# Optimization experiments

Measured on AMD Instinct MI355X. Metric: run time of the kernel, lower is better.

Reference implementation:

```python
import jax, jax.numpy as jnp
import numpy as np


def setup_inputs() -> dict:
    key = jax.random.key(0)
    ks = jax.random.split(key, 9)
    B, Cr, H, W = 16, 1024, 28, 28
    Cs, Hs, Ws = 256, 25, 25  # Hs == Ws so adaptive pool == mean over width
    Ci = 512
    return {
        "x_rgb": jax.random.normal(ks[0], (B, Cr, H, W), jnp.float32),
        "x_skel": jax.random.normal(ks[1], (B, Cs, Hs, Ws), jnp.float32),
        "Wq": jax.random.normal(ks[2], (Ci, Cr), jnp.float32) * (Cr ** -0.5),
        "bq": jax.random.normal(ks[3], (Ci,), jnp.float32) * 0.01,
        "Wk": jax.random.normal(ks[4], (Ci, Cs), jnp.float32) * (Cs ** -0.5),
        "bk": jax.random.normal(ks[5], (Ci,), jnp.float32) * 0.01,
        "Wv": jax.random.normal(ks[6], (Cr, Cs), jnp.float32) * (Cs ** -0.5),
        "bv": jax.random.normal(ks[7], (Cr,), jnp.float32) * 0.01,
        "gamma": jax.random.normal(ks[8], (1,), jnp.float32) * 0.1,
    }


def reference(x_rgb, x_skel, Wq, bq, Wk, bk, Wv, bv, gamma):
    B, Cr, H, W = x_rgb.shape
    Ws = x_skel.shape[3]
    # adaptive_avg_pool2d(x_skel, (Ws, 1)) with Hs == Ws -> mean over width
    pooled = jnp.mean(x_skel, axis=3)  # [B, Cs, Ws]
    # 1x1 conv projections as matmuls
    q = jnp.einsum('ic,bchw->bihw', Wq, x_rgb) + bq[None, :, None, None]
    q = q.reshape(B, -1, H * W).transpose(0, 2, 1)          # [B, HW, Ci]
    k = jnp.einsum('ic,bcs->bis', Wk, pooled) + bk[None, :, None]  # [B, Ci, Ws]
    energy = jnp.einsum('bni,bis->bns', q, k)               # [B, HW, Ws]
    attention = jax.nn.softmax(energy, axis=-1)             # [B, HW, Ws]
    v = jnp.einsum('rc,bcs->brs', Wv, pooled) + bv[None, :, None]  # [B, Cr, Ws]
    out = jnp.einsum('brs,bns->brn', v, attention)          # [B, Cr, HW]
    out = out.reshape(B, Cr, H, W)
    return gamma[0] * out + x_rgb
```

## Files before the change

kernel.cpp:

```cpp
#include <hip/hip_runtime.h>

#define BB 16
#define CR 1024
#define HWD 784
#define HW2 392
#define CS 256
#define SSZ 25
#define SP 28
#define CI 512
#define CSPLIT 8
#define CCHUNK 128
#define RSPLIT 32
#define RCHUNK 32
#define KC 4

#define OFF_POOLED 0
#define OFF_VP     102400
#define OFF_MP     561152
#define OFF_E0     1019904
#define OFF_ATT    1020304
#define OFF_EP     1333904
#define OFF_KK     1333904
#define OFF_P      1563280

__global__ __launch_bounds__(256) void k_pool(const float* __restrict__ xs,
                                              float* __restrict__ pooled) {
    __shared__ float buf[4][400];
    int wave = threadIdx.x >> 6, lane = threadIdx.x & 63;
    int r0 = blockIdx.x * 64 + wave * 16;
    const float4* src = (const float4*)(xs + (size_t)r0 * SSZ);
    float4* b4 = (float4*)buf[wave];
    b4[lane] = src[lane];
    if (lane < 36) b4[64 + lane] = src[64 + lane];
    __syncthreads();
    if (lane < 16) {
        const float* row = buf[wave] + lane * SSZ;
        float s = 0.f;
#pragma unroll
        for (int w = 0; w < SSZ; ++w) s += row[w];
        pooled[r0 + lane] = s * (1.0f / SSZ);
    }
}

template <int NS>
__device__ __forceinline__ void proj_body(const float* __restrict__ wrow,
                                          const float* __restrict__ pb, int s0,
                                          float bias, float* __restrict__ dst,
                                          bool zpad) {
    float acc[NS];
#pragma unroll
    for (int i = 0; i < NS; ++i) acc[i] = 0.f;
    const float4* w4 = (const float4*)wrow;
#pragma unroll 4
    for (int c4 = 0; c4 < CS / 4; ++c4) {
        float4 w = w4[c4];
        const float* p = pb + c4 * 4 * SSZ + s0;
#pragma unroll
        for (int i = 0; i < NS; ++i)
            acc[i] = fmaf(w.x, p[i],
                     fmaf(w.y, p[SSZ + i],
                     fmaf(w.z, p[2 * SSZ + i],
                     fmaf(w.w, p[3 * SSZ + i], acc[i]))));
    }
#pragma unroll
    for (int i = 0; i < NS; ++i) dst[s0 + i] = acc[i] + bias;
    if (zpad) { dst[25] = 0.f; dst[26] = 0.f; dst[27] = 0.f; }
}

__global__ __launch_bounds__(256) void k_kkv(const float* __restrict__ Wk,
                                             const float* __restrict__ Wv,
                                             const float* __restrict__ bk,
                                             const float* __restrict__ bv,
                                             const float* __restrict__ pooled,
                                             float* __restrict__ kk,
                                             float* __restrict__ vp) {
    int rb = blockIdx.x >> 2, sh = blockIdx.x & 3;
    int b = blockIdx.y;
    const float* pb = pooled + (size_t)b * CS * SSZ;
    const float* wrow;
    float bias;
    float* dst;
    if (rb < 2) {
        int i = rb * 256 + threadIdx.x;
        wrow = Wk + (size_t)i * CS;
        bias = bk[i];
        dst = kk + ((size_t)b * CI + i) * SP;
    } else {
        int r = (rb - 2) * 256 + threadIdx.x;
        wrow = Wv + (size_t)r * CS;
        bias = bv[r];
        dst = vp + ((size_t)b * CR + r) * SP;
    }
    int s0 = sh * 7;
    if (sh < 3) proj_body<7>(wrow, pb, s0, bias, dst, false);
    else        proj_body<4>(wrow, pb, s0, bias, dst, true);
}

__global__ __launch_bounds__(256) void k_Mpart(const float* __restrict__ Wq,
                                               const float* __restrict__ kk,
                                               float* __restrict__ P) {
    __shared__ __align__(16) float lds[128 * 8];
    int sh = blockIdx.x, kc = blockIdx.y, b = blockIdx.z;
    int t = threadIdx.x;
    int s0 = sh * 7;
    int i0 = kc * 128;
    const float* kkb = kk + (size_t)b * CI * SP;
#pragma unroll
    for (int q = 0; q < 4; ++q) {
        int d = t + 256 * q;
        lds[d] = kkb[(size_t)(i0 + (d >> 3)) * SP + s0 + (d & 7)];
    }
    __syncthreads();

    float acc[28];
#pragma unroll
    for (int e = 0; e < 28; ++e) acc[e] = 0.f;
    const float4* lds4 = (const float4*)lds;
#pragma unroll 4
    for (int i = 0; i < 128; ++i) {
        float4 w = *(const float4*)(Wq + (size_t)(i0 + i) * CR + 4 * t);
        float4 k0 = lds4[i * 2];
        float4 k1 = lds4[i * 2 + 1];
#pragma unroll
        for (int j = 0; j < 4; ++j) {
            float wj = j == 0 ? w.x : j == 1 ? w.y : j == 2 ? w.z : w.w;
            acc[j * 7 + 0] = fmaf(wj, k0.x, acc[j * 7 + 0]);
            acc[j * 7 + 1] = fmaf(wj, k0.y, acc[j * 7 + 1]);
            acc[j * 7 + 2] = fmaf(wj, k0.z, acc[j * 7 + 2]);
            acc[j * 7 + 3] = fmaf(wj, k0.w, acc[j * 7 + 3]);
            acc[j * 7 + 4] = fmaf(wj, k1.x, acc[j * 7 + 4]);
            acc[j * 7 + 5] = fmaf(wj, k1.y, acc[j * 7 + 5]);
            acc[j * 7 + 6] = fmaf(wj, k1.z, acc[j * 7 + 6]);
        }
    }
    float* dst = P + ((((size_t)kc * BB + b) * 4 + sh) * 256 + t) * 28;
#pragma unroll
    for (int m = 0; m < 7; ++m) {
        float4 o;
        o.x = acc[4 * m + 0]; o.y = acc[4 * m + 1];
        o.z = acc[4 * m + 2]; o.w = acc[4 * m + 3];
        *(float4*)(dst + 4 * m) = o;
    }
}

__global__ __launch_bounds__(256) void k_Mred(const float* __restrict__ P,
                                              float* __restrict__ Mp) {
    int id = blockIdx.x * 256 + threadIdx.x;
    int t = id & 255, sh = (id >> 8) & 3, b = id >> 10;
    const float* p0 = P + ((((size_t)b) * 4 + sh) * 256 + t) * 28;
    const size_t PL = (size_t)BB * 4 * 256 * 28;
    float v[28];
#pragma unroll
    for (int m = 0; m < 7; ++m) {
        float4 a = *(const float4*)(p0 + 4 * m);
        float4 b1 = *(const float4*)(p0 + PL + 4 * m);
        float4 c = *(const float4*)(p0 + 2 * PL + 4 * m);
        float4 d = *(const float4*)(p0 + 3 * PL + 4 * m);
        v[4 * m + 0] = a.x + b1.x + c.x + d.x;
        v[4 * m + 1] = a.y + b1.y + c.y + d.y;
        v[4 * m + 2] = a.z + b1.z + c.z + d.z;
        v[4 * m + 3] = a.w + b1.w + c.w + d.w;
    }
    int s0 = sh * 7;
    float* mb = Mp + ((size_t)b * CR + 4 * t) * SP + s0;
#pragma unroll
    for (int j = 0; j < 4; ++j)
#pragma unroll
        for (int u = 0; u < 7; ++u)
            mb[j * SP + u] = v[j * 7 + u];
}

__global__ __launch_bounds__(64) void k_e0(const float* __restrict__ bq,
                                           const float* __restrict__ kk,
                                           float* __restrict__ e0) {
    int s = blockIdx.x, b = blockIdx.y;
    int l = threadIdx.x;
    const float* kb = kk + (size_t)b * CI * SP;
    float a = 0.f;
#pragma unroll
    for (int k = 0; k < CI / 64; ++k) {
        int i = l + 64 * k;
        a = fmaf(bq[i], kb[(size_t)i * SP + s], a);
    }
#pragma unroll
    for (int off = 32; off > 0; off >>= 1) a += __shfl_down(a, off);
    if (l == 0) e0[b * SSZ + s] = a;
}

__global__ __launch_bounds__(64) void k_energy(const float* __restrict__ xr,
                                               const float* __restrict__ Mp,
                                               float* __restrict__ Ep) {
    __shared__ float ldsM[CCHUNK * SP];
    int lane = threadIdx.x;
    int b = blockIdx.y, ch = blockIdx.z;
    int cbeg = ch * CCHUNK;
    {
        const float4* src = (const float4*)(Mp + ((size_t)b * CR + cbeg) * SP);
        float4* dst = (float4*)ldsM;
#pragma unroll
        for (int j = 0; j < 14; ++j) dst[lane + 64 * j] = src[lane + 64 * j];
    }
    __syncthreads();

    int n2 = blockIdx.x * 64 + lane;
    bool valid = n2 < HW2;
    int n2c = valid ? n2 : 0;
    const float2* x2 = (const float2*)(xr + (size_t)b * CR * HWD);

    float acc0[SP], acc1[SP];
#pragma unroll
    for (int s = 0; s < SP; ++s) { acc0[s] = 0.f; acc1[s] = 0.f; }

    for (int c = 0; c < CCHUNK; c += 4) {
        float2 xv[4];
#pragma unroll
        for (int u = 0; u < 4; ++u)
            xv[u] = x2[(size_t)(cbeg + c + u) * HW2 + n2c];
#pragma unroll
        for (int u = 0; u < 4; ++u) {
            const float4* mr = (const float4*)&ldsM[(c + u) * SP];
#pragma unroll
            for (int j = 0; j < 7; ++j) {
                float4 m = mr[j];
                acc0[4 * j + 0] = fmaf(xv[u].x, m.x, acc0[4 * j + 0]);
                acc0[4 * j + 1] = fmaf(xv[u].x, m.y, acc0[4 * j + 1]);
                acc0[4 * j + 2] = fmaf(xv[u].x, m.z, acc0[4 * j + 2]);
                acc0[4 * j + 3] = fmaf(xv[u].x, m.w, acc0[4 * j + 3]);
                acc1[4 * j + 0] = fmaf(xv[u].y, m.x, acc1[4 * j + 0]);
                acc1[4 * j + 1] = fmaf(xv[u].y, m.y, acc1[4 * j + 1]);
                acc1[4 * j + 2] = fmaf(xv[u].y, m.z, acc1[4 * j + 2]);
                acc1[4 * j + 3] = fmaf(xv[u].y, m.w, acc1[4 * j + 3]);
            }
        }
    }
    if (valid) {
        float2* ep = (float2*)Ep + ((size_t)(ch * BB + b) * SSZ) * HW2 + n2;
#pragma unroll
        for (int s = 0; s < SSZ; ++s) ep[(size_t)s * HW2] = make_float2(acc0[s], acc1[s]);
    }
}

__global__ __launch_bounds__(64) void k_softmax(const float* __restrict__ Ep,
                                                const float* __restrict__ e0,
                                                float* __restrict__ att) {
    int lane = threadIdx.x;
    int n2 = blockIdx.x * 64 + lane;
    int b = blockIdx.y;
    if (n2 >= HW2) return;
    float ex[SSZ], ey[SSZ];
#pragma unroll
    for (int s = 0; s < SSZ; ++s) { float v = e0[b * SSZ + s]; ex[s] = v; ey[s] = v; }
    const float2* ep2 = (const float2*)Ep;
    for (int ch = 0; ch < CSPLIT; ++ch) {
        const float2* ep = ep2 + ((size_t)(ch * BB + b) * SSZ) * HW2 + n2;
#pragma unroll
        for (int s = 0; s < SSZ; ++s) {
            float2 v = ep[(size_t)s * HW2];
            ex[s] += v.x; ey[s] += v.y;
        }
    }
    float mx = ex[0], my = ey[0];
#pragma unroll
    for (int s = 1; s < SSZ; ++s) { mx = fmaxf(mx, ex[s]); my = fmaxf(my, ey[s]); }
    float sx = 0.f, sy = 0.f;
#pragma unroll
    for (int s = 0; s < SSZ; ++s) {
        ex[s] = __expf(ex[s] - mx); sx += ex[s];
        ey[s] = __expf(ey[s] - my); sy += ey[s];
    }
    float ix = 1.0f / sx, iy = 1.0f / sy;
    float2* ao = (float2*)att + ((size_t)b * SSZ) * HW2 + n2;
#pragma unroll
    for (int s = 0; s < SSZ; ++s) ao[(size_t)s * HW2] = make_float2(ex[s] * ix, ey[s] * iy);
}

__global__ __launch_bounds__(64) void k_out(const float* __restrict__ xr,
                                            const float* __restrict__ vp,
                                            const float* __restrict__ att,
                                            const float* __restrict__ gamma,
                                            float* __restrict__ out) {
    __shared__ float ldsv[RCHUNK * SP];
    int lane = threadIdx.x;
    int b = blockIdx.y, rz = blockIdx.z;
    int r0 = rz * RCHUNK;
    {
        const float4* src = (const float4*)(vp + ((size_t)b * CR + r0) * SP);
        float4* dst = (float4*)ldsv;
#pragma unroll
        for (int j = 0; j < 4; ++j) {
            int idx = lane + 64 * j;
            if (idx < RCHUNK * SP / 4) dst[idx] = src[idx];
        }
    }
    __syncthreads();

    int n2 = blockIdx.x * 64 + lane;
    bool valid = n2 < HW2;
    int n2c = valid ? n2 : 0;

    float a0[SP], a1[SP];
    const float2* at2 = (const float2*)att + ((size_t)b * SSZ) * HW2 + n2c;
#pragma unroll
    for (int s = 0; s < SSZ; ++s) {
        float2 av = at2[(size_t)s * HW2];
        a0[s] = av.x; a1[s] = av.y;
    }
#pragma unroll
    for (int s = SSZ; s < SP; ++s) { a0[s] = 0.f; a1[s] = 0.f; }

    float g = gamma[0];
    const float2* x2 = (const float2*)(xr + (size_t)b * CR * HWD);
    float2* o2 = (float2*)(out + (size_t)b * CR * HWD);

#pragma unroll 4
    for (int r = 0; r < RCHUNK; ++r) {
        float2 xv = x2[(size_t)(r0 + r) * HW2 + n2c];
        float d0 = 0.f, d1 = 0.f;
        const float4* vr = (const float4*)&ldsv[r * SP];
#pragma unroll
        for (int j = 0; j < 7; ++j) {
            float4 v = vr[j];
            d0 = fmaf(v.x, a0[4 * j + 0], d0);
            d0 = fmaf(v.y, a0[4 * j + 1], d0);
            d0 = fmaf(v.z, a0[4 * j + 2], d0);
            d0 = fmaf(v.w, a0[4 * j + 3], d0);
            d1 = fmaf(v.x, a1[4 * j + 0], d1);
            d1 = fmaf(v.y, a1[4 * j + 1], d1);
            d1 = fmaf(v.z, a1[4 * j + 2], d1);
            d1 = fmaf(v.w, a1[4 * j + 3], d1);
        }
        if (valid)
            o2[(size_t)(r0 + r) * HW2 + n2] = make_float2(fmaf(g, d0, xv.x), fmaf(g, d1, xv.y));
    }
}

extern "C" void kernel_launch(void* const* d_in, const int* in_sizes, int n_in,
                              void* d_out, int out_size, void* d_ws, size_t ws_size,
                              hipStream_t stream) {
    const float* x_rgb  = (const float*)d_in[0];
    const float* x_skel = (const float*)d_in[1];
    const float* Wq     = (const float*)d_in[2];
    const float* bq     = (const float*)d_in[3];
    const float* Wk     = (const float*)d_in[4];
    const float* bk     = (const float*)d_in[5];
    const float* Wv     = (const float*)d_in[6];
    const float* bv     = (const float*)d_in[7];
    const float* gamma  = (const float*)d_in[8];
    float* out = (float*)d_out;

    float* ws     = (float*)d_ws;
    float* pooled = ws + OFF_POOLED;
    float* vp     = ws + OFF_VP;
    float* Mp     = ws + OFF_MP;
    float* e0     = ws + OFF_E0;
    float* att    = ws + OFF_ATT;
    float* Ep     = ws + OFF_EP;
    float* kk     = ws + OFF_KK;
    float* P      = ws + OFF_P;

    k_pool   <<<dim3(1600),           256, 0, stream>>>(x_skel, pooled);
    k_kkv    <<<dim3(24, 16),         256, 0, stream>>>(Wk, Wv, bk, bv, pooled, kk, vp);
    k_Mpart  <<<dim3(4, KC, 16),      256, 0, stream>>>(Wq, kk, P);
    k_Mred   <<<dim3(64),             256, 0, stream>>>(P, Mp);
    k_e0     <<<dim3(25, 16),          64, 0, stream>>>(bq, kk, e0);
    k_energy <<<dim3(7, 16, CSPLIT),   64, 0, stream>>>(x_rgb, Mp, Ep);
    k_softmax<<<dim3(7, 16),           64, 0, stream>>>(Ep, e0, att);
    k_out    <<<dim3(7, 16, RSPLIT),   64, 0, stream>>>(x_rgb, vp, att, gamma, out);
}
```

Measured before the change: 241.3 us.

## Fuse all stages into one persistent kernel with software grid barriers

Replaces eight separate kernel launches with a single 1024-block kernel that runs each stage in turn and separates them with an atomic-counter grid barrier. The aim is to remove per-launch overhead and the idle gaps between small dependent kernels. Blocks change from 64 to 256 threads for the energy and output stages, and the pooling stage now reads rows directly without staging them in LDS. In exchange, every block must spin at each barrier, the barrier is only correct if all 1024 blocks are resident at once, and its bounded spin can exit early and break ordering.

```diff
diff --git a/kernel.cpp b/kernel.cpp
--- a/kernel.cpp
+++ b/kernel.cpp
@@ -10,9 +10,9 @@
 #define CI 512
 #define CSPLIT 8
 #define CCHUNK 128
-#define RSPLIT 32
 #define RCHUNK 32
 #define KC 4
+#define NBLK 1024
 
 #define OFF_POOLED 0
 #define OFF_VP     102400
@@ -22,24 +22,26 @@
 #define OFF_EP     1333904
 #define OFF_KK     1333904
 #define OFF_P      1563280
-
-__global__ __launch_bounds__(256) void k_pool(const float* __restrict__ xs,
-                                              float* __restrict__ pooled) {
-    __shared__ float buf[4][400];
-    int wave = threadIdx.x >> 6, lane = threadIdx.x & 63;
-    int r0 = blockIdx.x * 64 + wave * 16;
-    const float4* src = (const float4*)(xs + (size_t)r0 * SSZ);
-    float4* b4 = (float4*)buf[wave];
-    b4[lane] = src[lane];
-    if (lane < 36) b4[64 + lane] = src[64 + lane];
+#define OFF_BAR    3842704
+
+__device__ __forceinline__ void gbar(unsigned* bar) {
     __syncthreads();
-    if (lane < 16) {
-        const float* row = buf[wave] + lane * SSZ;
-        float s = 0.f;
-#pragma unroll
-        for (int w = 0; w < SSZ; ++w) s += row[w];
-        pooled[r0 + lane] = s * (1.0f / SSZ);
-    }
+    if (threadIdx.x == 0) {
+        unsigned g = __hip_atomic_load(bar + 1, __ATOMIC_RELAXED, __HIP_MEMORY_SCOPE_AGENT);
+        unsigned a = __hip_atomic_fetch_add(bar, 1u, __ATOMIC_ACQ_REL, __HIP_MEMORY_SCOPE_AGENT);
+        if (a == (unsigned)(NBLK - 1)) {
+            __hip_atomic_store(bar, 0u, __ATOMIC_RELAXED, __HIP_MEMORY_SCOPE_AGENT);
+            __hip_atomic_fetch_add(bar + 1, 1u, __ATOMIC_RELEASE, __HIP_MEMORY_SCOPE_AGENT);
+        } else {
+            int spins = 0;
+            while (__hip_atomic_load(bar + 1, __ATOMIC_RELAXED, __HIP_MEMORY_SCOPE_AGENT) == g) {
+                __builtin_amdgcn_s_sleep(1);
+                if (++spins > (1 << 22)) break;
+            }
+        }
+        __threadfence();
+    }
+    __syncthreads();
 }
 
 template <int NS>
@@ -67,270 +69,281 @@
     if (zpad) { dst[25] = 0.f; dst[26] = 0.f; dst[27] = 0.f; }
 }
 
-__global__ __launch_bounds__(256) void k_kkv(const float* __restrict__ Wk,
-                                             const float* __restrict__ Wv,
-                                             const float* __restrict__ bk,
-                                             const float* __restrict__ bv,
-                                             const float* __restrict__ pooled,
-                                             float* __restrict__ kk,
-                                             float* __restrict__ vp) {
-    int rb = blockIdx.x >> 2, sh = blockIdx.x & 3;
-    int b = blockIdx.y;
-    const float* pb = pooled + (size_t)b * CS * SSZ;
-    const float* wrow;
-    float bias;
-    float* dst;
-    if (rb < 2) {
-        int i = rb * 256 + threadIdx.x;
-        wrow = Wk + (size_t)i * CS;
-        bias = bk[i];
-        dst = kk + ((size_t)b * CI + i) * SP;
-    } else {
-        int r = (rb - 2) * 256 + threadIdx.x;
-        wrow = Wv + (size_t)r * CS;
-        bias = bv[r];
-        dst = vp + ((size_t)b * CR + r) * SP;
-    }
-    int s0 = sh * 7;
-    if (sh < 3) proj_body<7>(wrow, pb, s0, bias, dst, false);
-    else        proj_body<4>(wrow, pb, s0, bias, dst, true);
-}
-
-__global__ __launch_bounds__(256) void k_Mpart(const float* __restrict__ Wq,
-                                               const float* __restrict__ kk,
-                                               float* __restrict__ P) {
-    __shared__ __align__(16) float lds[128 * 8];
-    int sh = blockIdx.x, kc = blockIdx.y, b = blockIdx.z;
-    int t = threadIdx.x;
-    int s0 = sh * 7;
-    int i0 = kc * 128;
-    const float* kkb = kk + (size_t)b * CI * SP;
-#pragma unroll
-    for (int q = 0; q < 4; ++q) {
-        int d = t + 256 * q;
-        lds[d] = kkb[(size_t)(i0 + (d >> 3)) * SP + s0 + (d & 7)];
-    }
-    __syncthreads();
-
-    float acc[28];
-#pragma unroll
-    for (int e = 0; e < 28; ++e) acc[e] = 0.f;
-    const float4* lds4 = (const float4*)lds;
+__global__ __launch_bounds__(256, 4) void mega(
+    const float* __restrict__ xr, const float* __restrict__ xs,
+    const float* __restrict__ Wq, const float* __restrict__ bq,
+    const float* __restrict__ Wk, const float* __restrict__ bk,
+    const float* __restrict__ Wv, const float* __restrict__ bv,
+    const float* __restrict__ gm, float* __restrict__ out,
+    float* __restrict__ ws)
+{
+    __shared__ __align__(16) float lds[CCHUNK * SP];
+
+    float* pooled = ws + OFF_POOLED;
+    float* vp     = ws + OFF_VP;
+    float* Mp     = ws + OFF_MP;
+    float* e0     = ws + OFF_E0;
+    float* att    = ws + OFF_ATT;
+    float* Ep     = ws + OFF_EP;
+    float* kk     = ws + OFF_KK;
+    float* P      = ws + OFF_P;
+    unsigned* bar = (unsigned*)(ws + OFF_BAR);
+
+    const int tid  = threadIdx.x;
+    const int wave = tid >> 6, lane = tid & 63;
+    const int bid  = blockIdx.x;
+
+    {
+        int id = bid * 256 + tid;
+        if (id < BB * CS * SSZ) {
+            const float* row = xs + (size_t)id * SSZ;
+            float s = 0.f;
+#pragma unroll
+            for (int w = 0; w < SSZ; ++w) s += row[w];
+            pooled[id] = s * (1.0f / SSZ);
+        }
+    }
+    gbar(bar);
+
+    if (bid < 24 * BB) {
+        int xx = bid % 24, b = bid / 24;
+        int rb = xx >> 2, sh = xx & 3;
+        const float* pb = pooled + (size_t)b * CS * SSZ;
+        const float* wrow; float bias; float* dst;
+        if (rb < 2) {
+            int i = rb * 256 + tid;
+            wrow = Wk + (size_t)i * CS; bias = bk[i];
+            dst  = kk + ((size_t)b * CI + i) * SP;
+        } else {
+            int r = (rb - 2) * 256 + tid;
+            wrow = Wv + (size_t)r * CS; bias = bv[r];
+            dst  = vp + ((size_t)b * CR + r) * SP;
+        }
+        int s0 = sh * 7;
+        if (sh < 3) proj_body<7>(wrow, pb, s0, bias, dst, false);
+        else        proj_body<4>(wrow, pb, s0, bias, dst, true);
+    }
+    gbar(bar);
+
+    if (bid < 4 * KC * BB) {
+        int sh = bid & 3, kc = (bid >> 2) & 3, b = bid >> 4;
+        int s0 = sh * 7, i0 = kc * 128;
+        const float* kkb = kk + (size_t)b * CI * SP;
+#pragma unroll
+        for (int q = 0; q < 4; ++q) {
+            int d = tid + 256 * q;
+            lds[d] = kkb[(size_t)(i0 + (d >> 3)) * SP + s0 + (d & 7)];
+        }
+        __syncthreads();
+        float acc[28];
+#pragma unroll
+        for (int e = 0; e < 28; ++e) acc[e] = 0.f;
+        const float4* lds4 = (const float4*)lds;
 #pragma unroll 4
-    for (int i = 0; i < 128; ++i) {
-        float4 w = *(const float4*)(Wq + (size_t)(i0 + i) * CR + 4 * t);
-        float4 k0 = lds4[i * 2];
-        float4 k1 = lds4[i * 2 + 1];
-#pragma unroll
-        for (int j = 0; j < 4; ++j) {
-            float wj = j == 0 ? w.x : j == 1 ? w.y : j == 2 ? w.z : w.w;
-            acc[j * 7 + 0] = fmaf(wj, k0.x, acc[j * 7 + 0]);
-            acc[j * 7 + 1] = fmaf(wj, k0.y, acc[j * 7 + 1]);
-            acc[j * 7 + 2] = fmaf(wj, k0.z, acc[j * 7 + 2]);
-            acc[j * 7 + 3] = fmaf(wj, k0.w, acc[j * 7 + 3]);
-            acc[j * 7 + 4] = fmaf(wj, k1.x, acc[j * 7 + 4]);
-            acc[j * 7 + 5] = fmaf(wj, k1.y, acc[j * 7 + 5]);
-            acc[j * 7 + 6] = fmaf(wj, k1.z, acc[j * 7 + 6]);
-        }
-    }
-    float* dst = P + ((((size_t)kc * BB + b) * 4 + sh) * 256 + t) * 28;
-#pragma unroll
-    for (int m = 0; m < 7; ++m) {
-        float4 o;
-        o.x = acc[4 * m + 0]; o.y = acc[4 * m + 1];
-        o.z = acc[4 * m + 2]; o.w = acc[4 * m + 3];
-        *(float4*)(dst + 4 * m) = o;
-    }
-}
-
-__global__ __launch_bounds__(256) void k_Mred(const float* __restrict__ P,
-                                              float* __restrict__ Mp) {
-    int id = blockIdx.x * 256 + threadIdx.x;
-    int t = id & 255, sh = (id >> 8) & 3, b = id >> 10;
-    const float* p0 = P + ((((size_t)b) * 4 + sh) * 256 + t) * 28;
-    const size_t PL = (size_t)BB * 4 * 256 * 28;
-    float v[28];
-#pragma unroll
-    for (int m = 0; m < 7; ++m) {
-        float4 a = *(const float4*)(p0 + 4 * m);
-        float4 b1 = *(const float4*)(p0 + PL + 4 * m);
-        float4 c = *(const float4*)(p0 + 2 * PL + 4 * m);
-        float4 d = *(const float4*)(p0 + 3 * PL + 4 * m);
-        v[4 * m + 0] = a.x + b1.x + c.x + d.x;
-        v[4 * m + 1] = a.y + b1.y + c.y + d.y;
-        v[4 * m + 2] = a.z + b1.z + c.z + d.z;
-        v[4 * m + 3] = a.w + b1.w + c.w + d.w;
-    }
-    int s0 = sh * 7;
-    float* mb = Mp + ((size_t)b * CR + 4 * t) * SP + s0;
-#pragma unroll
-    for (int j = 0; j < 4; ++j)
-#pragma unroll
-        for (int u = 0; u < 7; ++u)
-            mb[j * SP + u] = v[j * 7 + u];
-}
-
-__global__ __launch_bounds__(64) void k_e0(const float* __restrict__ bq,
-                                           const float* __restrict__ kk,
-                                           float* __restrict__ e0) {
-    int s = blockIdx.x, b = blockIdx.y;
-    int l = threadIdx.x;
-    const float* kb = kk + (size_t)b * CI * SP;
-    float a = 0.f;
-#pragma unroll
-    for (int k = 0; k < CI / 64; ++k) {
-        int i = l + 64 * k;
-        a = fmaf(bq[i], kb[(size_t)i * SP + s], a);
-    }
-#pragma unroll
-    for (int off = 32; off > 0; off >>= 1) a += __shfl_down(a, off);
-    if (l == 0) e0[b * SSZ + s] = a;
-}
-
-__global__ __launch_bounds__(64) void k_energy(const float* __restrict__ xr,
-                                               const float* __restrict__ Mp,
-                                               float* __restrict__ Ep) {
-    __shared__ float ldsM[CCHUNK * SP];
-    int lane = threadIdx.x;
-    int b = blockIdx.y, ch = blockIdx.z;
-    int cbeg = ch * CCHUNK;
+        for (int i = 0; i < 128; ++i) {
+            float4 w = *(const float4*)(Wq + (size_t)(i0 + i) * CR + 4 * tid);
+            float4 k0 = lds4[i * 2];
+            float4 k1 = lds4[i * 2 + 1];
+#pragma unroll
+            for (int j = 0; j < 4; ++j) {
+                float wj = j == 0 ? w.x : j == 1 ? w.y : j == 2 ? w.z : w.w;
+                acc[j * 7 + 0] = fmaf(wj, k0.x, acc[j * 7 + 0]);
+                acc[j * 7 + 1] = fmaf(wj, k0.y, acc[j * 7 + 1]);
+                acc[j * 7 + 2] = fmaf(wj, k0.z, acc[j * 7 + 2]);
+                acc[j * 7 + 3] = fmaf(wj, k0.w, acc[j * 7 + 3]);
+                acc[j * 7 + 4] = fmaf(wj, k1.x, acc[j * 7 + 4]);
+                acc[j * 7 + 5] = fmaf(wj, k1.y, acc[j * 7 + 5]);
+                acc[j * 7 + 6] = fmaf(wj, k1.z, acc[j * 7 + 6]);
+            }
+        }
+        float* dstP = P + ((((size_t)kc * BB + b) * 4 + sh) * 256 + tid) * 28;
+#pragma unroll
+        for (int m = 0; m < 7; ++m) {
+            float4 o;
+            o.x = acc[4 * m + 0]; o.y = acc[4 * m + 1];
+            o.z = acc[4 * m + 2]; o.w = acc[4 * m + 3];
+            *(float4*)(dstP + 4 * m) = o;
+        }
+    }
+    gbar(bar);
+
+    if (bid < 64) {
+        int id = bid * 256 + tid;
+        int t = id & 255, sh = (id >> 8) & 3, b = id >> 10;
+        const float* p0 = P + ((((size_t)b) * 4 + sh) * 256 + t) * 28;
+        const size_t PL = (size_t)BB * 4 * 256 * 28;
+        float vv[28];
+#pragma unroll
+        for (int m = 0; m < 7; ++m) {
+            float4 a  = *(const float4*)(p0 + 4 * m);
+            float4 b1 = *(const float4*)(p0 + PL + 4 * m);
+            float4 c  = *(const float4*)(p0 + 2 * PL + 4 * m);
+            float4 d  = *(const float4*)(p0 + 3 * PL + 4 * m);
+            vv[4 * m + 0] = a.x + b1.x + c.x + d.x;
+            vv[4 * m + 1] = a.y + b1.y + c.y + d.y;
+            vv[4 * m + 2] = a.z + b1.z + c.z + d.z;
+            vv[4 * m + 3] = a.w + b1.w + c.w + d.w;
+        }
+        int s0 = sh * 7;
+        float* mb = Mp + ((size_t)b * CR + 4 * t) * SP + s0;
+#pragma unroll
+        for (int j = 0; j < 4; ++j)
+#pragma unroll
+            for (int u = 0; u < 7; ++u)
+                mb[j * SP + u] = vv[j * 7 + u];
+    } else if (bid < 164) {
+        int wtask = (bid - 64) * 4 + wave;
+        int s = wtask % 25, b = wtask / 25;
+        const float* kb = kk + (size_t)b * CI * SP;
+        float a = 0.f;
+#pragma unroll
+        for (int k = 0; k < CI / 64; ++k) {
+            int i = lane + 64 * k;
+            a = fmaf(bq[i], kb[(size_t)i * SP + s], a);
+        }
+#pragma unroll
+        for (int off = 32; off > 0; off >>= 1) a += __shfl_down(a, off);
+        if (lane == 0) e0[b * SSZ + s] = a;
+    }
+    gbar(bar);
+
+    if (bid < 2 * CSPLIT * BB) {
+        int nq = bid & 1, ch = (bid >> 1) & 7, b = bid >> 4;
+        int cbeg = ch * CCHUNK;
+        {
+            const float4* src = (const float4*)(Mp + ((size_t)b * CR + cbeg) * SP);
+            float4* dst = (float4*)lds;
+#pragma unroll
+            for (int j = 0; j < 4; ++j) {
+                int idx = tid + 256 * j;
+                if (idx < CCHUNK * SP / 4) dst[idx] = src[idx];
+            }
+        }
+        __syncthreads();
+        int u = nq * 4 + wave;
+        if (u < 7) {
+            int n2 = u * 64 + lane;
+            bool valid = n2 < HW2;
+            int n2c = valid ? n2 : 0;
+            const float2* x2 = (const float2*)(xr + (size_t)b * CR * HWD);
+            float acc0[SP], acc1[SP];
+#pragma unroll
+            for (int s = 0; s < SP; ++s) { acc0[s] = 0.f; acc1[s] = 0.f; }
+            for (int c = 0; c < CCHUNK; c += 8) {
+                float2 xv[8];
+#pragma unroll
+                for (int q = 0; q < 8; ++q)
+                    xv[q] = x2[(size_t)(cbeg + c + q) * HW2 + n2c];
+#pragma unroll
+                for (int q = 0; q < 8; ++q) {
+                    const float4* mr = (const float4*)&lds[(c + q) * SP];
+#pragma unroll
+                    for (int j = 0; j < 7; ++j) {
+                        float4 m = mr[j];
+                        acc0[4 * j + 0] = fmaf(xv[q].x, m.x, acc0[4 * j + 0]);
+                        acc0[4 * j + 1] = fmaf(xv[q].x, m.y, acc0[4 * j + 1]);
+                        acc0[4 * j + 2] = fmaf(xv[q].x, m.z, acc0[4 * j + 2]);
+                        acc0[4 * j + 3] = fmaf(xv[q].x, m.w, acc0[4 * j + 3]);
+                        acc1[4 * j + 0] = fmaf(xv[q].y, m.x, acc1[4 * j + 0]);
+                        acc1[4 * j + 1] = fmaf(xv[q].y, m.y, acc1[4 * j + 1]);
+                        acc1[4 * j + 2] = fmaf(xv[q].y, m.z, acc1[4 * j + 2]);
+                        acc1[4 * j + 3] = fmaf(xv[q].y, m.w, acc1[4 * j + 3]);
+                    }
+                }
+            }
+            if (valid) {
+                float2* ep = (float2*)Ep + ((size_t)(ch * BB + b) * SSZ) * HW2 + n2;
+#pragma unroll
+                for (int s = 0; s < SSZ; ++s)
+                    ep[(size_t)s * HW2] = make_float2(acc0[s], acc1[s]);
+            }
+        }
+    }
+    gbar(bar);
+
+    if (bid < 28) {
+        int wtask = bid * 4 + wave;
+        int nb = wtask % 7, b = wtask / 7;
+        int n2 = nb * 64 + lane;
+        if (n2 < HW2) {
+            float ex[SSZ], ey[SSZ];
+#pragma unroll
+            for (int s = 0; s < SSZ; ++s) { float v = e0[b * SSZ + s]; ex[s] = v; ey[s] = v; }
+            const float2* ep2 = (const float2*)Ep;
+            for (int ch = 0; ch < CSPLIT; ++ch) {
+                const float2* ep = ep2 + ((size_t)(ch * BB + b) * SSZ) * HW2 + n2;
+#pragma unroll
+                for (int s = 0; s < SSZ; ++s) {
+                    float2 v = ep[(size_t)s * HW2];
+                    ex[s] += v.x; ey[s] += v.y;
+                }
+            }
+            float mx = ex[0], my = ey[0];
+#pragma unroll
+            for (int s = 1; s < SSZ; ++s) { mx = fmaxf(mx, ex[s]); my = fmaxf(my, ey[s]); }
+            float sx = 0.f, sy = 0.f;
+#pragma unroll
+            for (int s = 0; s < SSZ; ++s) {
+                ex[s] = __expf(ex[s] - mx); sx += ex[s];
+                ey[s] = __expf(ey[s] - my); sy += ey[s];
+            }
+            float ix = 1.0f / sx, iy = 1.0f / sy;
+            float2* ao = (float2*)att + ((size_t)b * SSZ) * HW2 + n2;
+#pragma unroll
+            for (int s = 0; s < SSZ; ++s)
+                ao[(size_t)s * HW2] = make_float2(ex[s] * ix, ey[s] * iy);
+        }
+    }
+    gbar(bar);
+
     {
-        const float4* src = (const float4*)(Mp + ((size_t)b * CR + cbeg) * SP);
-        float4* dst = (float4*)ldsM;
-#pragma unroll
-        for (int j = 0; j < 14; ++j) dst[lane + 64 * j] = src[lane + 64 * j];
-    }
-    __syncthreads();
-
-    int n2 = blockIdx.x * 64 + lane;
-    bool valid = n2 < HW2;
-    int n2c = valid ? n2 : 0;
-    const float2* x2 = (const float2*)(xr + (size_t)b * CR * HWD);
-
-    float acc0[SP], acc1[SP];
-#pragma unroll
-    for (int s = 0; s < SP; ++s) { acc0[s] = 0.f; acc1[s] = 0.f; }
-
-    for (int c = 0; c < CCHUNK; c += 4) {
-        float2 xv[4];
-#pragma unroll
-        for (int u = 0; u < 4; ++u)
-            xv[u] = x2[(size_t)(cbeg + c + u) * HW2 + n2c];
-#pragma unroll
-        for (int u = 0; u < 4; ++u) {
-            const float4* mr = (const float4*)&ldsM[(c + u) * SP];
-#pragma unroll
-            for (int j = 0; j < 7; ++j) {
-                float4 m = mr[j];
-                acc0[4 * j + 0] = fmaf(xv[u].x, m.x, acc0[4 * j + 0]);
-                acc0[4 * j + 1] = fmaf(xv[u].x, m.y, acc0[4 * j + 1]);
-                acc0[4 * j + 2] = fmaf(xv[u].x, m.z, acc0[4 * j + 2]);
-                acc0[4 * j + 3] = fmaf(xv[u].x, m.w, acc0[4 * j + 3]);
-                acc1[4 * j + 0] = fmaf(xv[u].y, m.x, acc1[4 * j + 0]);
-                acc1[4 * j + 1] = fmaf(xv[u].y, m.y, acc1[4 * j + 1]);
-                acc1[4 * j + 2] = fmaf(xv[u].y, m.z, acc1[4 * j + 2]);
-                acc1[4 * j + 3] = fmaf(xv[u].y, m.w, acc1[4 * j + 3]);
-            }
-        }
-    }
-    if (valid) {
-        float2* ep = (float2*)Ep + ((size_t)(ch * BB + b) * SSZ) * HW2 + n2;
-#pragma unroll
-        for (int s = 0; s < SSZ; ++s) ep[(size_t)s * HW2] = make_float2(acc0[s], acc1[s]);
-    }
-}
-
-__global__ __launch_bounds__(64) void k_softmax(const float* __restrict__ Ep,
-                                                const float* __restrict__ e0,
-                                                float* __restrict__ att) {
-    int lane = threadIdx.x;
-    int n2 = blockIdx.x * 64 + lane;
-    int b = blockIdx.y;
-    if (n2 >= HW2) return;
-    float ex[SSZ], ey[SSZ];
-#pragma unroll
-    for (int s = 0; s < SSZ; ++s) { float v = e0[b * SSZ + s]; ex[s] = v; ey[s] = v; }
-    const float2* ep2 = (const float2*)Ep;
-    for (int ch = 0; ch < CSPLIT; ++ch) {
-        const float2* ep = ep2 + ((size_t)(ch * BB + b) * SSZ) * HW2 + n2;
-#pragma unroll
-        for (int s = 0; s < SSZ; ++s) {
-            float2 v = ep[(size_t)s * HW2];
-            ex[s] += v.x; ey[s] += v.y;
-        }
-    }
-    float mx = ex[0], my = ey[0];
-#pragma unroll
-    for (int s = 1; s < SSZ; ++s) { mx = fmaxf(mx, ex[s]); my = fmaxf(my, ey[s]); }
-    float sx = 0.f, sy = 0.f;
-#pragma unroll
-    for (int s = 0; s < SSZ; ++s) {
-        ex[s] = __expf(ex[s] - mx); sx += ex[s];
-        ey[s] = __expf(ey[s] - my); sy += ey[s];
-    }
-    float ix = 1.0f / sx, iy = 1.0f / sy;
-    float2* ao = (float2*)att + ((size_t)b * SSZ) * HW2 + n2;
-#pragma unroll
-    for (int s = 0; s < SSZ; ++s) ao[(size_t)s * HW2] = make_float2(ex[s] * ix, ey[s] * iy);
-}
-
-__global__ __launch_bounds__(64) void k_out(const float* __restrict__ xr,
-                                            const float* __restrict__ vp,
-                                            const float* __restrict__ att,
-                                            const float* __restrict__ gamma,
-                                            float* __restrict__ out) {
-    __shared__ float ldsv[RCHUNK * SP];
-    int lane = threadIdx.x;
-    int b = blockIdx.y, rz = blockIdx.z;
-    int r0 = rz * RCHUNK;
-    {
-        const float4* src = (const float4*)(vp + ((size_t)b * CR + r0) * SP);
-        float4* dst = (float4*)ldsv;
-#pragma unroll
-        for (int j = 0; j < 4; ++j) {
-            int idx = lane + 64 * j;
-            if (idx < RCHUNK * SP / 4) dst[idx] = src[idx];
-        }
-    }
-    __syncthreads();
-
-    int n2 = blockIdx.x * 64 + lane;
-    bool valid = n2 < HW2;
-    int n2c = valid ? n2 : 0;
-
-    float a0[SP], a1[SP];
-    const float2* at2 = (const float2*)att + ((size_t)b * SSZ) * HW2 + n2c;
-#pragma unroll
-    for (int s = 0; s < SSZ; ++s) {
-        float2 av = at2[(size_t)s * HW2];
-        a0[s] = av.x; a1[s] = av.y;
-    }
-#pragma unroll
-    for (int s = SSZ; s < SP; ++s) { a0[s] = 0.f; a1[s] = 0.f; }
-
-    float g = gamma[0];
-    const float2* x2 = (const float2*)(xr + (size_t)b * CR * HWD);
-    float2* o2 = (float2*)(out + (size_t)b * CR * HWD);
-
+        int nq = bid & 1, rz = (bid >> 1) & 31, b = bid >> 6;
+        int r0 = rz * RCHUNK;
+        {
+            const float4* src = (const float4*)(vp + ((size_t)b * CR + r0) * SP);
+            float4* dst = (float4*)lds;
+            if (tid < RCHUNK * SP / 4) dst[tid] = src[tid];
+        }
+        __syncthreads();
+        int u = nq * 4 + wave;
+        if (u < 7) {
+            int n2 = u * 64 + lane;
+            bool valid = n2 < HW2;
+            int n2c = valid ? n2 : 0;
+            float a0[SP], a1[SP];
+            const float2* at2 = (const float2*)att + ((size_t)b * SSZ) * HW2 + n2c;
+#pragma unroll
+            for (int s = 0; s < SSZ; ++s) {
+                float2 av = at2[(size_t)s * HW2];
+                a0[s] = av.x; a1[s] = av.y;
+            }
+#pragma unroll
+            for (int s = SSZ; s < SP; ++s) { a0[s] = 0.f; a1[s] = 0.f; }
+            float g = gm[0];
+            const float2* x2 = (const float2*)(xr + (size_t)b * CR * HWD);
+            float2* o2 = (float2*)(out + (size_t)b * CR * HWD);
 #pragma unroll 4
-    for (int r = 0; r < RCHUNK; ++r) {
-        float2 xv = x2[(size_t)(r0 + r) * HW2 + n2c];
-        float d0 = 0.f, d1 = 0.f;
-        const float4* vr = (const float4*)&ldsv[r * SP];
-#pragma unroll
-        for (int j = 0; j < 7; ++j) {
-            float4 v = vr[j];
-            d0 = fmaf(v.x, a0[4 * j + 0], d0);
-            d0 = fmaf(v.y, a0[4 * j + 1], d0);
-            d0 = fmaf(v.z, a0[4 * j + 2], d0);
-            d0 = fmaf(v.w, a0[4 * j + 3], d0);
-            d1 = fmaf(v.x, a1[4 * j + 0], d1);
-            d1 = fmaf(v.y, a1[4 * j + 1], d1);
-            d1 = fmaf(v.z, a1[4 * j + 2], d1);
-            d1 = fmaf(v.w, a1[4 * j + 3], d1);
-        }
-        if (valid)
-            o2[(size_t)(r0 + r) * HW2 + n2] = make_float2(fmaf(g, d0, xv.x), fmaf(g, d1, xv.y));
+            for (int r = 0; r < RCHUNK; ++r) {
+                float2 xv = x2[(size_t)(r0 + r) * HW2 + n2c];
+                float d0 = 0.f, d1 = 0.f;
+                const float4* vr = (const float4*)&lds[r * SP];
+#pragma unroll
+                for (int j = 0; j < 7; ++j) {
+                    float4 v = vr[j];
+                    d0 = fmaf(v.x, a0[4 * j + 0], d0);
+                    d0 = fmaf(v.y, a0[4 * j + 1], d0);
+                    d0 = fmaf(v.z, a0[4 * j + 2], d0);
+                    d0 = fmaf(v.w, a0[4 * j + 3], d0);
+                    d1 = fmaf(v.x, a1[4 * j + 0], d1);
+                    d1 = fmaf(v.y, a1[4 * j + 1], d1);
+                    d1 = fmaf(v.z, a1[4 * j + 2], d1);
+                    d1 = fmaf(v.w, a1[4 * j + 3], d1);
+                }
+                if (valid)
+                    o2[(size_t)(r0 + r) * HW2 + n2] =
+                        make_float2(fmaf(g, d0, xv.x), fmaf(g, d1, xv.y));
+            }
+        }
     }
 }
 
@@ -347,23 +360,10 @@
     const float* bv     = (const float*)d_in[7];
     const float* gamma  = (const float*)d_in[8];
     float* out = (float*)d_out;
-
-    float* ws     = (float*)d_ws;
-    float* pooled = ws + OFF_POOLED;
-    float* vp     = ws + OFF_VP;
-    float* Mp     = ws + OFF_MP;
-    float* e0     = ws + OFF_E0;
-    float* att    = ws + OFF_ATT;
-    float* Ep     = ws + OFF_EP;
-    float* kk     = ws + OFF_KK;
-    float* P      = ws + OFF_P;
-
-    k_pool   <<<dim3(1600),           256, 0, stream>>>(x_skel, pooled);
-    k_kkv    <<<dim3(24, 16),         256, 0, stream>>>(Wk, Wv, bk, bv, pooled, kk, vp);
-    k_Mpart  <<<dim3(4, KC, 16),      256, 0, stream>>>(Wq, kk, P);
-    k_Mred   <<<dim3(64),             256, 0, stream>>>(P, Mp);
-    k_e0     <<<dim3(25, 16),          64, 0, stream>>>(bq, kk, e0);
-    k_energy <<<dim3(7, 16, CSPLIT),   64, 0, stream>>>(x_rgb, Mp, Ep);
-    k_softmax<<<dim3(7, 16),           64, 0, stream>>>(Ep, e0, att);
-    k_out    <<<dim3(7, 16, RSPLIT),   64, 0, stream>>>(x_rgb, vp, att, gamma, out);
+    float* ws  = (float*)d_ws;
+
+    hipMemsetAsync(ws + OFF_BAR, 0, 2 * sizeof(unsigned), stream);
+
+    hipLaunchKernelGGL(mega, dim3(NBLK), dim3(256), 0, stream,
+                       x_rgb, x_skel, Wq, bq, Wk, bk, Wv, bv, gamma, out, ws);
 }
```

After: 742.4 us. 3.08x slower.
